# Kernel tuning notes

Measured on AMD Instinct MI355X. Metric: run time of the kernel, lower is better.

## Reference

```python
import jax, jax.numpy as jnp
import numpy as np

NH = 16          # num_attention_heads
SMAX = 400.0     # smax for previous-task gates

def _gelu(x):
    return jax.nn.gelu(x, approximate=False)

def setup_inputs() -> dict:
    key = jax.random.key(0)
    ks = jax.random.split(key, 18)
    B, S, H, A, N = 8, 2048, 1024, 512, 10
    sc = lambda fan: 1.0 / np.sqrt(fan)
    f32 = jnp.float32
    return {
        "x":     jax.random.normal(ks[0], (B, S, H), f32),
        "fc1_w": jax.random.normal(ks[1], (A, H), f32) * sc(H),
        "fc1_b": jnp.zeros((A,), f32),
        "fc2_w": jax.random.normal(ks[2], (H, A), f32) * sc(A),
        "fc2_b": jnp.zeros((H,), f32),
        "efc1":  jax.random.normal(ks[3], (N, A), f32),
        "efc2":  jax.random.normal(ks[4], (N, H), f32),
        "etask": jax.random.normal(ks[5], (N, H), f32),
        "q_w":   jax.random.normal(ks[6], (H, H), f32) * sc(H),
        "q_b":   jnp.zeros((H,), f32),
        "k_w":   jax.random.normal(ks[7], (H, H), f32) * sc(H),
        "k_b":   jnp.zeros((H,), f32),
        "v_w":   jax.random.normal(ks[8], (H, H), f32) * sc(H),
        "v_b":   jnp.zeros((H,), f32),
        "equery": jax.random.normal(ks[9],  (N, H), f32),
        "ekey":   jax.random.normal(ks[10], (N, H), f32),
        "evalue": jax.random.normal(ks[11], (N, H), f32),
        "t": 5,
        "s": 400,
    }

def reference(x, fc1_w, fc1_b, fc2_w, fc2_b, efc1, efc2, etask,
              q_w, q_b, k_w, k_b, v_w, v_b, equery, ekey, evalue, t, s):
    B, S, H = x.shape
    hd = H // NH
    s = jnp.float32(s)

    # --- current-task gated adapter: h = act(fc2(act(fc1(x)) * gfc1)) * gfc2 ---
    h1 = _gelu(x @ fc1_w.T + fc1_b)                         # [B,S,A]
    gfc1 = jax.nn.sigmoid(s * efc1[t])                      # [A]
    gfc2 = jax.nn.sigmoid(s * efc2[t])                      # [H]
    h = _gelu((h1 * gfc1) @ fc2_w.T + fc2_b) * gfc2         # [B,S,H]

    # --- previous tasks (detached, gates at smax); vectorized over pre_t ---
    pg1 = jax.nn.sigmoid(SMAX * efc1[:t])                   # [t,A]
    pg2 = jax.nn.sigmoid(SMAX * efc2[:t])                   # [t,H]
    pre_h1 = h1[:, None, :, :] * pg1[None, :, None, :]      # [B,t,S,A]
    pre_h = _gelu(jnp.einsum('btsa,ha->btsh', pre_h1, fc2_w) + fc2_b)
    pre_h = jax.lax.stop_gradient(pre_h * pg2[None, :, None, :])  # [B,t,S,H]

    hid = jnp.concatenate([h[:, None], pre_h], axis=1)      # [B,T,S,H], T=t+1
    Tn = t + 1

    # --- task-gated QKV ---
    t_emb = jnp.broadcast_to(etask[t], (B, 1, S, H))        # query_states
    gq = jax.nn.sigmoid(s * equery[t])
    gk = jax.nn.sigmoid(s * ekey[t])
    gv = jax.nn.sigmoid(s * evalue[t])
    q = (t_emb @ q_w.T + q_b) * gq                          # [B,1,S,H]
    k = (hid @ k_w.T + k_b) * gk                            # [B,T,S,H]
    v = (hid @ v_w.T + v_b) * gv                            # [B,T,S,H]

    q5 = q.reshape(B, 1, S, NH, hd)
    k5 = k.reshape(B, Tn, S, NH, hd)
    v5 = v.reshape(B, Tn, S, NH, hd)

    # torch permute algebra: contract over heads (n), softmax over tasks (t)
    scores = jnp.einsum('bqsnd,btsnd->bdsqt', q5, k5) / np.sqrt(hd)  # [B,hd,S,1,T]
    probs = jax.nn.softmax(scores, axis=-1)
    ctx = jnp.einsum('bdsqt,btsnd->bdsqn', probs, v5)       # [B,hd,S,1,NH]
    ctx = ctx[:, :, :, 0, :].transpose(0, 2, 1, 3).reshape(B, S, H)

    return x + ctx
```

## Files before the change

kernel.cpp:

```cpp
#include <hip/hip_runtime.h>
#include <hip/hip_bf16.h>

static constexpr int B_ = 8, S_ = 2048, H_ = 1024, A_ = 512;
static constexpr int M_ = B_ * S_;
static constexpr int T_ = 6;
static constexpr long HID_STRIDE = (long)M_ * H_;
static constexpr long SC_STRIDE  = (long)M_ * 64;

typedef __attribute__((ext_vector_type(4))) float f32x4;
typedef __attribute__((ext_vector_type(8))) short bf16x8;

__device__ __forceinline__ float bf2f(ushort u){ return __uint_as_float(((unsigned)u) << 16); }
__device__ __forceinline__ ushort f2bf(float f){
  __hip_bfloat16 h = __float2bfloat16(f);
  return __builtin_bit_cast(unsigned short, h);
}
__device__ __forceinline__ float geluf(float x){
  return 0.5f * x * (1.0f + erff(x * 0.70710678118654752440f));
}
__device__ __forceinline__ float sigm(float x){ return 1.0f / (1.0f + __expf(-x)); }

__device__ __forceinline__ void gload_lds16(const void* g, void* l){
  __builtin_amdgcn_global_load_lds((const __attribute__((address_space(1))) void*)g,
                                   (__attribute__((address_space(3))) void*)l, 16, 0, 0);
}


__global__ void gates_kernel(const float* __restrict__ efc1, const float* __restrict__ efc2,
                             const int* __restrict__ tptr, const int* __restrict__ sptr,
                             float* __restrict__ g1, float* __restrict__ g2)
{
  const int h = threadIdx.x;
  const int t = *tptr;
  const float s = (float)(*sptr);
  #pragma unroll
  for (int ti = 0; ti < T_; ++ti) {
    const int task = (ti == 0) ? t : (ti - 1);
    const float scl = (ti == 0) ? s : 400.0f;
    g2[ti * H_ + h] = sigm(scl * efc2[task * H_ + h]);
    if (h < A_) g1[ti * A_ + h] = sigm(scl * efc1[task * A_ + h]);
  }
}

__global__ void kq_kernel(const float* __restrict__ etask, const float* __restrict__ q_w,
                          const float* __restrict__ q_b, const float* __restrict__ equery,
                          const float* __restrict__ ekey, const float* __restrict__ k_w,
                          const float* __restrict__ k_b,
                          const int* __restrict__ tptr, const int* __restrict__ sptr,
                          ushort* __restrict__ kqw, float* __restrict__ kqb)
{
  __shared__ float qg[16];
  const int d = blockIdx.x;
  const int tid = threadIdx.x;
  const int t = *tptr;
  const float s = (float)(*sptr);
  if (tid < 16) {
    const int hp = tid * 64 + d;
    const float* et = etask + (long)t * H_;
    const float* qw = q_w + (long)hp * H_;
    float acc = 0.f;
    for (int i = 0; i < H_; ++i) acc += et[i] * qw[i];
    float qv = (acc + q_b[hp]) * sigm(s * equery[t * H_ + hp]);
    qg[tid] = qv * sigm(s * ekey[t * H_ + hp]);
  }
  __syncthreads();
  for (int hh = tid; hh < H_; hh += 256) {
    float acc = 0.f;
    #pragma unroll
    for (int n = 0; n < 16; ++n) acc += qg[n] * k_w[(long)(n * 64 + d) * H_ + hh];
    kqw[d * H_ + hh] = f2bf(acc);
  }
  if (tid == 0) {
    float acc = 0.f;
    #pragma unroll
    for (int n = 0; n < 16; ++n) acc += qg[n] * k_b[n * 64 + d];
    kqb[d] = acc;
  }
}

__global__ void conv_bf16(const float* __restrict__ in, ushort* __restrict__ outp, long n)
{
  long i = ((long)blockIdx.x * blockDim.x + threadIdx.x) * 4;
  const long stride = (long)gridDim.x * blockDim.x * 4;
  for (; i < n; i += stride) {
    float4 v = *(const float4*)(in + i);
    ushort4 o;
    o.x = f2bf(v.x); o.y = f2bf(v.y); o.z = f2bf(v.z); o.w = f2bf(v.w);
    *(ushort4*)(outp + i) = o;
  }
}

__global__ void conv_w2g(const float* __restrict__ fc2w, const float* __restrict__ g1,
                         ushort* __restrict__ W2g)
{
  const long total = (long)T_ * H_ * A_;
  long i = ((long)blockIdx.x * blockDim.x + threadIdx.x) * 4;
  if (i >= total) return;
  const int ti = (int)(i / ((long)H_ * A_));
  const long r = i - (long)ti * H_ * A_;
  const int a = (int)(r & (A_ - 1));
  float4 wv = *(const float4*)(fc2w + r);
  const float* g = g1 + ti * A_ + a;
  ushort4 o;
  o.x = f2bf(wv.x * g[0]); o.y = f2bf(wv.y * g[1]);
  o.z = f2bf(wv.z * g[2]); o.w = f2bf(wv.w * g[3]);
  *(ushort4*)(W2g + i) = o;
}

__global__ void conv_vw(const float* __restrict__ v_w, const float* __restrict__ v_b,
                        const float* __restrict__ evalue,
                        const int* __restrict__ tptr, const int* __restrict__ sptr,
                        ushort* __restrict__ vwb, float* __restrict__ vbg)
{
  const int t = *tptr;
  const float s = (float)(*sptr);
  long i = ((long)blockIdx.x * blockDim.x + threadIdx.x) * 4;
  if (i < (long)H_ * H_) {
    const int f = (int)(i >> 10);
    const int hp = ((f & 15) << 6) + (f >> 4);
    const float g = sigm(s * evalue[t * H_ + hp]);
    float4 wv = *(const float4*)(v_w + ((long)hp << 10) + (i & 1023));
    ushort4 o;
    o.x = f2bf(wv.x * g); o.y = f2bf(wv.y * g);
    o.z = f2bf(wv.z * g); o.w = f2bf(wv.w * g);
    *(ushort4*)(vwb + i) = o;
  }
  const long j = (long)blockIdx.x * blockDim.x + threadIdx.x;
  if (j < H_) {
    const int hp = (((int)j & 15) << 6) + ((int)j >> 4);
    vbg[j] = v_b[hp] * sigm(s * evalue[t * H_ + hp]);
  }
}

template<int BM, int BN, int EPI>
__global__ __launch_bounds__(256)
void gemm_bt(const ushort* __restrict__ A, const ushort* __restrict__ Bm,
             void* __restrict__ C, const float* __restrict__ bias,
             const float* __restrict__ scale,
             int M, int N, int K,
             long strideAz, long strideBz, long strideCz, int strideSz,
             float postmul)
{
  constexpr int BK = 32;
  constexpr int WM = BM / 2, WN = BN / 2;
  constexpr int MI = WM / 16, NI = WN / 16;
  constexpr int L = BM / 64 + BN / 64;
  __shared__ alignas(16) ushort As[3][BM * BK];
  __shared__ alignas(16) ushort Bs[3][BN * BK];

  const int z = blockIdx.z;
  A  += (long)z * strideAz;
  Bm += (long)z * strideBz;

  const int gx = gridDim.x, gy = gridDim.y;
  int flat = blockIdx.y * gx + blockIdx.x;
  const int nwg = gx * gy;
  if ((nwg & 7) == 0) flat = (flat & 7) * (nwg >> 3) + (flat >> 3);
  const int m0 = (flat / gy) * BM, n0 = (flat % gy) * BN;

  const int tid = threadIdx.x, lane = tid & 63, wid = tid >> 6;
  const int wr = wid >> 1, wc = wid & 1;
  const int srow = tid >> 2;
  const int scol = (tid & 3) * 8;
  const int scol_src = (((tid & 3) ^ ((tid >> 3) & 3))) * 8;

  auto stage = [&](int buf, int kk) {
    #pragma unroll
    for (int i = 0; i < BM / 64; ++i)
      gload_lds16(A + (long)(m0 + i * 64 + srow) * K + kk + scol_src,
                  &As[buf][(i * 64 + srow) * BK + scol]);
    #pragma unroll
    for (int i = 0; i < BN / 64; ++i)
      gload_lds16(Bm + (long)(n0 + i * 64 + srow) * K + kk + scol_src,
                  &Bs[buf][(i * 64 + srow) * BK + scol]);
  };

  f32x4 acc[MI][NI] = {};
  const int NT = K / BK;
  const int ks = (((lane >> 4) ^ ((lane >> 1) & 3))) * 8;

  stage(0, 0);
  stage(1, BK);

  int cur = 0;
  for (int t = 0; t < NT; ++t) {
    if (t + 1 < NT) {
      if constexpr (L == 4) asm volatile("s_waitcnt vmcnt(4)" ::: "memory");
      else                  asm volatile("s_waitcnt vmcnt(3)" ::: "memory");
    } else {
      asm volatile("s_waitcnt vmcnt(0)" ::: "memory");
    }
    __builtin_amdgcn_s_barrier();
    __builtin_amdgcn_sched_barrier(0);

    bf16x8 af[MI], bfr[NI];
    #pragma unroll
    for (int m = 0; m < MI; ++m)
      af[m] = *(const bf16x8*)&As[cur][(wr * WM + m * 16 + (lane & 15)) * BK + ks];
    #pragma unroll
    for (int n = 0; n < NI; ++n)
      bfr[n] = *(const bf16x8*)&Bs[cur][(wc * WN + n * 16 + (lane & 15)) * BK + ks];
    __builtin_amdgcn_sched_barrier(0);

    if (t + 2 < NT) {
      int nb = cur + 2; if (nb >= 3) nb -= 3;
      stage(nb, (t + 2) * BK);
    }

    asm volatile("s_waitcnt lgkmcnt(0)" ::: "memory");
    __builtin_amdgcn_sched_barrier(0);

    __builtin_amdgcn_s_setprio(1);
    #pragma unroll
    for (int m = 0; m < MI; ++m)
      #pragma unroll
      for (int n = 0; n < NI; ++n)
        acc[m][n] = __builtin_amdgcn_mfma_f32_16x16x32_bf16(af[m], bfr[n], acc[m][n], 0, 0, 0);
    __builtin_amdgcn_s_setprio(0);
    ++cur; if (cur >= 3) cur = 0;
  }

  const float* sc = (EPI == 1) ? (scale + (long)z * strideSz) : nullptr;
  #pragma unroll
  for (int m = 0; m < MI; ++m) {
    #pragma unroll
    for (int n = 0; n < NI; ++n) {
      const int col = n0 + wc * WN + n * 16 + (lane & 15);
      const float bv = bias[col];
      #pragma unroll
      for (int r = 0; r < 4; ++r) {
        const int row = m0 + wr * WM + m * 16 + (lane >> 4) * 4 + r;
        const float v = acc[m][n][r] + bv;
        const long ci = (long)z * strideCz + (long)row * N + col;
        if constexpr (EPI == 0) {
          ((ushort*)C)[ci] = f2bf(geluf(v));
        } else if constexpr (EPI == 1) {
          ((ushort*)C)[ci] = f2bf(geluf(v) * sc[col]);
        } else {
          ((float*)C)[ci] = v * postmul;
        }
      }
    }
  }
}

__global__ __launch_bounds__(256)
void fusedv_kernel(const ushort* __restrict__ hidb, const ushort* __restrict__ vwb,
                   const float* __restrict__ scB, const float* __restrict__ vbg,
                   const float* __restrict__ x, float* __restrict__ out)
{
  constexpr int BM = 128, BN = 128, BK = 32;
  constexpr int WM = 64, WN = 64, MI = 4, NI = 4;
  constexpr int NT = T_ * 32;
  __shared__ alignas(16) ushort As[3][BM * BK];
  __shared__ alignas(16) ushort Bs[3][BN * BK];
  __shared__ alignas(16) float p_lds[T_ * BM * 8];

  const int gx = gridDim.x, gy = gridDim.y;
  int flat = blockIdx.y * gx + blockIdx.x;
  const int nwg = gx * gy;
  flat = (flat & 7) * (nwg >> 3) + (flat >> 3);
  const int m0 = (flat / gy) * BM, n0 = (flat % gy) * BN;
  const int d0 = n0 >> 4;

  const int tid = threadIdx.x, lane = tid & 63, wid = tid >> 6;
  const int wr = wid >> 1, wc = wid & 1;
  const int srow = tid >> 2;
  const int scol = (tid & 3) * 8;
  const int scol_src = (((tid & 3) ^ ((tid >> 3) & 3))) * 8;
  const int ks = (((lane >> 4) ^ ((lane >> 1) & 3))) * 8;

  auto stageAB = [&](int buf, int kt) {
    const int ti = kt >> 5;
    const int kk = (kt & 31) << 5;
    const ushort* Ap = hidb + (long)ti * HID_STRIDE;
    #pragma unroll
    for (int i = 0; i < 2; ++i)
      gload_lds16(Ap + (long)(m0 + i * 64 + srow) * H_ + kk + scol_src,
                  &As[buf][(i * 64 + srow) * BK + scol]);
    #pragma unroll
    for (int i = 0; i < 2; ++i)
      gload_lds16(vwb + (long)(n0 + i * 64 + srow) * H_ + kk + scol_src,
                  &Bs[buf][(i * 64 + srow) * BK + scol]);
  };

  stageAB(0, 0);
  #pragma unroll
  for (int c = 0; c < 4; ++c) {
    const int cell = tid + c * 256;
    const int row = cell >> 3, dl = cell & 7;
    const long base = (long)(m0 + row) * 64 + d0 + dl;
    float v[T_]; float mx = -1e30f;
    #pragma unroll
    for (int ti = 0; ti < T_; ++ti) {
      v[ti] = scB[(long)ti * SC_STRIDE + base];
      mx = fmaxf(mx, v[ti]);
    }
    float sum = 0.f;
    #pragma unroll
    for (int ti = 0; ti < T_; ++ti) { v[ti] = __expf(v[ti] - mx); sum += v[ti]; }
    const float inv = 1.0f / sum;
    #pragma unroll
    for (int ti = 0; ti < T_; ++ti) p_lds[(ti * BM + row) * 8 + dl] = v[ti] * inv;
  }
  asm volatile("s_waitcnt lgkmcnt(0)" ::: "memory");
  stageAB(1, 1);

  const f32x4 zero = {};
  f32x4 ctx[MI][NI] = {};
  f32x4 acc[MI][NI] = {};

  int cur = 0;
  for (int kt = 0; kt < NT; ++kt) {
    if (kt + 1 < NT) asm volatile("s_waitcnt vmcnt(4)" ::: "memory");
    else             asm volatile("s_waitcnt vmcnt(0)" ::: "memory");
    __builtin_amdgcn_s_barrier();
    __builtin_amdgcn_sched_barrier(0);

    bf16x8 af[MI], bfr[NI];
    #pragma unroll
    for (int m = 0; m < MI; ++m)
      af[m] = *(const bf16x8*)&As[cur][(wr * WM + m * 16 + (lane & 15)) * BK + ks];
    #pragma unroll
    for (int n = 0; n < NI; ++n)
      bfr[n] = *(const bf16x8*)&Bs[cur][(wc * WN + n * 16 + (lane & 15)) * BK + ks];
    __builtin_amdgcn_sched_barrier(0);

    if (kt + 2 < NT) {
      int nb = cur + 2; if (nb >= 3) nb -= 3;
      stageAB(nb, kt + 2);
    }

    asm volatile("s_waitcnt lgkmcnt(0)" ::: "memory");
    __builtin_amdgcn_sched_barrier(0);

    __builtin_amdgcn_s_setprio(1);
    #pragma unroll
    for (int m = 0; m < MI; ++m)
      #pragma unroll
      for (int n = 0; n < NI; ++n)
        acc[m][n] = __builtin_amdgcn_mfma_f32_16x16x32_bf16(af[m], bfr[n], acc[m][n], 0, 0, 0);
    __builtin_amdgcn_s_setprio(0);

    if ((kt & 31) == 31) {
      const int ti = kt >> 5;
      #pragma unroll
      for (int m = 0; m < MI; ++m) {
        #pragma unroll
        for (int r = 0; r < 4; ++r) {
          const int rowl = wr * WM + m * 16 + (lane >> 4) * 4 + r;
          const f32x4 pv = *(const f32x4*)&p_lds[(ti * BM + rowl) * 8 + wc * 4];
          #pragma unroll
          for (int n = 0; n < NI; ++n)
            ctx[m][n][r] += pv[n] * acc[m][n][r];
        }
        #pragma unroll
        for (int n = 0; n < NI; ++n) acc[m][n] = zero;
      }
    }
    ++cur; if (cur >= 3) cur = 0;
  }

  #pragma unroll
  for (int m = 0; m < MI; ++m) {
    #pragma unroll
    for (int n = 0; n < NI; ++n) {
      const int col = n0 + wc * WN + n * 16 + (lane & 15);
      const float bv = vbg[col];
      #pragma unroll
      for (int r = 0; r < 4; ++r) {
        const int row = m0 + wr * WM + m * 16 + (lane >> 4) * 4 + r;
        const long ci = (long)row * H_ + col;
        out[ci] = x[ci] + ctx[m][n][r] + bv;
      }
    }
  }
}

extern "C" void kernel_launch(void* const* d_in, const int* in_sizes, int n_in,
                              void* d_out, int out_size, void* d_ws, size_t ws_size,
                              hipStream_t stream)
{
  const float* x      = (const float*)d_in[0];
  const float* fc1_w  = (const float*)d_in[1];
  const float* fc1_b  = (const float*)d_in[2];
  const float* fc2_w  = (const float*)d_in[3];
  const float* fc2_b  = (const float*)d_in[4];
  const float* efc1   = (const float*)d_in[5];
  const float* efc2   = (const float*)d_in[6];
  const float* etask  = (const float*)d_in[7];
  const float* q_w    = (const float*)d_in[8];
  const float* q_b    = (const float*)d_in[9];
  const float* k_w    = (const float*)d_in[10];
  const float* k_b    = (const float*)d_in[11];
  const float* v_w    = (const float*)d_in[12];
  const float* v_b    = (const float*)d_in[13];
  const float* equery = (const float*)d_in[14];
  const float* ekey   = (const float*)d_in[15];
  const float* evalue = (const float*)d_in[16];
  const int*   tptr   = (const int*)d_in[17];
  const int*   sptr   = (const int*)d_in[18];
  float* out = (float*)d_out;

  char* w = (char*)d_ws;
  ushort* hidb = (ushort*)w; w += (long)T_ * M_ * H_ * 2;
  char* regionA = w;         w += (long)M_ * H_ * 2;
  ushort* xb  = (ushort*)regionA;
  float*  scB = (float*)regionA;
  ushort* h1b  = (ushort*)w; w += (long)M_ * A_ * 2;
  ushort* w1b  = (ushort*)w; w += (long)A_ * H_ * 2;
  ushort* W2g  = (ushort*)w; w += (long)T_ * H_ * A_ * 2;
  ushort* vwb  = (ushort*)w; w += (long)H_ * H_ * 2;
  ushort* kqw  = (ushort*)w; w += (long)64 * H_ * 2;
  float*  kqb  = (float*)w;  w += 64 * 4;
  float*  g1   = (float*)w;  w += T_ * A_ * 4;
  float*  g2   = (float*)w;  w += T_ * H_ * 4;
  float*  vbg  = (float*)w;  w += H_ * 4;
  (void)ws_size; (void)in_sizes; (void)n_in; (void)out_size;

  gates_kernel<<<1, 1024, 0, stream>>>(efc1, efc2, tptr, sptr, g1, g2);
  kq_kernel<<<64, 256, 0, stream>>>(etask, q_w, q_b, equery, ekey, k_w, k_b,
                                    tptr, sptr, kqw, kqb);
  conv_vw<<<1024, 256, 0, stream>>>(v_w, v_b, evalue, tptr, sptr, vwb, vbg);

  conv_bf16<<<2048, 256, 0, stream>>>(x, xb, (long)M_ * H_);
  conv_bf16<<<256, 256, 0, stream>>>(fc1_w, w1b, (long)A_ * H_);
  conv_w2g<<<3072, 256, 0, stream>>>(fc2_w, g1, W2g);

  gemm_bt<128, 128, 0><<<dim3(M_ / 128, A_ / 128, 1), 256, 0, stream>>>(
      xb, w1b, h1b, fc1_b, nullptr, M_, A_, H_, 0, 0, 0, 0, 0.f);

  gemm_bt<128, 128, 1><<<dim3(M_ / 128, H_ / 128, T_), 256, 0, stream>>>(
      h1b, W2g, hidb, fc2_b, g2, M_, H_, A_,
      0, (long)H_ * A_, HID_STRIDE, H_, 0.f);

  gemm_bt<128, 64, 2><<<dim3(M_ / 128, 1, T_), 256, 0, stream>>>(
      hidb, kqw, scB, kqb, nullptr, M_, 64, H_,
      HID_STRIDE, 0, SC_STRIDE, 0, 0.125f);

  fusedv_kernel<<<dim3(M_ / 128, H_ / 128, 1), 256, 0, stream>>>(
      hidb, vwb, scB, vbg, x, out);
}
```

Before: 551.4 us.

## Load V weight fragments directly into registers, bypassing LDS in fused V kernel

The V-projection weight tile is no longer staged through shared memory. Each wave loads its B fragments straight from global memory into registers, double-buffered across an even/odd unrolled K loop, while A stays in a 3-stage LDS ring. This removes LDS traffic and footprint for B. In exchange, each B element is loaded redundantly by both row-waves, the vmcnt accounting becomes more delicate, and register pressure rises.

```diff
diff --git a/kernel.cpp b/kernel.cpp
--- a/kernel.cpp
+++ b/kernel.cpp
@@ -253,7 +253,6 @@
   constexpr int WM = 64, WN = 64, MI = 4, NI = 4;
   constexpr int NT = T_ * 32;
   __shared__ alignas(16) ushort As[3][BM * BK];
-  __shared__ alignas(16) ushort Bs[3][BN * BK];
   __shared__ alignas(16) float p_lds[T_ * BM * 8];
 
   const int gx = gridDim.x, gy = gridDim.y;
@@ -270,7 +269,7 @@
   const int scol_src = (((tid & 3) ^ ((tid >> 3) & 3))) * 8;
   const int ks = (((lane >> 4) ^ ((lane >> 1) & 3))) * 8;
 
-  auto stageAB = [&](int buf, int kt) {
+  auto stageA = [&](int buf, int kt) {
     const int ti = kt >> 5;
     const int kk = (kt & 31) << 5;
     const ushort* Ap = hidb + (long)ti * HID_STRIDE;
@@ -278,13 +277,22 @@
     for (int i = 0; i < 2; ++i)
       gload_lds16(Ap + (long)(m0 + i * 64 + srow) * H_ + kk + scol_src,
                   &As[buf][(i * 64 + srow) * BK + scol]);
-    #pragma unroll
-    for (int i = 0; i < 2; ++i)
-      gload_lds16(vwb + (long)(n0 + i * 64 + srow) * H_ + kk + scol_src,
-                  &Bs[buf][(i * 64 + srow) * BK + scol]);
   };
 
-  stageAB(0, 0);
+  const ushort* Bbase = vwb + (long)(n0 + wc * WN + (lane & 15)) * H_ + (lane >> 4) * 8;
+  auto loadB = [&](int kt, bf16x8* dst) {
+    const int kk = (kt & 31) << 5;
+    #pragma unroll
+    for (int n = 0; n < NI; ++n)
+      dst[n] = *(const bf16x8*)(Bbase + (long)n * 16 * H_ + kk);
+  };
+  auto readA = [&](int buf, bf16x8* af) {
+    #pragma unroll
+    for (int m = 0; m < MI; ++m)
+      af[m] = *(const bf16x8*)&As[buf][(wr * WM + m * 16 + (lane & 15)) * BK + ks];
+  };
+
+  stageA(0, 0);
   #pragma unroll
   for (int c = 0; c < 4; ++c) {
     const int cell = tid + c * 256;
@@ -304,46 +312,63 @@
     for (int ti = 0; ti < T_; ++ti) p_lds[(ti * BM + row) * 8 + dl] = v[ti] * inv;
   }
   asm volatile("s_waitcnt lgkmcnt(0)" ::: "memory");
-  stageAB(1, 1);
+  bf16x8 bEven[NI], bOdd[NI];
+  loadB(0, bEven);
+  stageA(1, 1);
 
   const f32x4 zero = {};
   f32x4 ctx[MI][NI] = {};
   f32x4 acc[MI][NI] = {};
 
   int cur = 0;
-  for (int kt = 0; kt < NT; ++kt) {
-    if (kt + 1 < NT) asm volatile("s_waitcnt vmcnt(4)" ::: "memory");
-    else             asm volatile("s_waitcnt vmcnt(0)" ::: "memory");
+  for (int t = 0; t < NT; t += 2) {
+    asm volatile("s_waitcnt vmcnt(6)" ::: "memory");
     __builtin_amdgcn_s_barrier();
     __builtin_amdgcn_sched_barrier(0);
 
-    bf16x8 af[MI], bfr[NI];
+    bf16x8 afA[MI];
+    readA(cur, afA);
+    __builtin_amdgcn_sched_barrier(0);
+    loadB(t + 1, bOdd);
+    {
+      int nb = cur + 2; if (nb >= 3) nb -= 3;
+      if (t + 2 < NT) stageA(nb, t + 2);
+    }
+    asm volatile("s_waitcnt lgkmcnt(0)" ::: "memory");
+    __builtin_amdgcn_sched_barrier(0);
+    __builtin_amdgcn_s_setprio(1);
     #pragma unroll
     for (int m = 0; m < MI; ++m)
-      af[m] = *(const bf16x8*)&As[cur][(wr * WM + m * 16 + (lane & 15)) * BK + ks];
-    #pragma unroll
-    for (int n = 0; n < NI; ++n)
-      bfr[n] = *(const bf16x8*)&Bs[cur][(wc * WN + n * 16 + (lane & 15)) * BK + ks];
-    __builtin_amdgcn_sched_barrier(0);
-
-    if (kt + 2 < NT) {
-      int nb = cur + 2; if (nb >= 3) nb -= 3;
-      stageAB(nb, kt + 2);
-    }
-
-    asm volatile("s_waitcnt lgkmcnt(0)" ::: "memory");
-    __builtin_amdgcn_sched_barrier(0);
-
-    __builtin_amdgcn_s_setprio(1);
-    #pragma unroll
-    for (int m = 0; m < MI; ++m)
       #pragma unroll
       for (int n = 0; n < NI; ++n)
-        acc[m][n] = __builtin_amdgcn_mfma_f32_16x16x32_bf16(af[m], bfr[n], acc[m][n], 0, 0, 0);
+        acc[m][n] = __builtin_amdgcn_mfma_f32_16x16x32_bf16(afA[m], bEven[n], acc[m][n], 0, 0, 0);
     __builtin_amdgcn_s_setprio(0);
 
-    if ((kt & 31) == 31) {
-      const int ti = kt >> 5;
+    {
+      int curO = cur + 1; if (curO >= 3) curO -= 3;
+      if (t + 2 < NT) asm volatile("s_waitcnt vmcnt(6)" ::: "memory");
+      else            asm volatile("s_waitcnt vmcnt(4)" ::: "memory");
+      __builtin_amdgcn_s_barrier();
+      __builtin_amdgcn_sched_barrier(0);
+
+      bf16x8 afB[MI];
+      readA(curO, afB);
+      __builtin_amdgcn_sched_barrier(0);
+      if (t + 2 < NT) loadB(t + 2, bEven);
+      if (t + 3 < NT) stageA(cur, t + 3);
+      asm volatile("s_waitcnt lgkmcnt(0)" ::: "memory");
+      __builtin_amdgcn_sched_barrier(0);
+      __builtin_amdgcn_s_setprio(1);
+      #pragma unroll
+      for (int m = 0; m < MI; ++m)
+        #pragma unroll
+        for (int n = 0; n < NI; ++n)
+          acc[m][n] = __builtin_amdgcn_mfma_f32_16x16x32_bf16(afB[m], bOdd[n], acc[m][n], 0, 0, 0);
+      __builtin_amdgcn_s_setprio(0);
+    }
+
+    if (((t + 1) & 31) == 31) {
+      const int ti = (t + 1) >> 5;
       #pragma unroll
       for (int m = 0; m < MI; ++m) {
         #pragma unroll
@@ -358,7 +383,7 @@
         for (int n = 0; n < NI; ++n) acc[m][n] = zero;
       }
     }
-    ++cur; if (cur >= 3) cur = 0;
+    cur += 2; if (cur >= 3) cur -= 3;
   }
 
   #pragma unroll
```

Result: slower. 852.8 us (+54.7%).
